# Performance work log

Measured on AMD Instinct MI355X. Metric: run time of the kernel, lower is better.

## Reference

```python
import jax, jax.numpy as jnp
import numpy as np

HIDDEN = 768
HEADS = 12
HEAD_DIM = HIDDEN // HEADS


def setup_inputs() -> dict:
    key = jax.random.key(0)
    ks = jax.random.split(key, 5)
    B, S = 1, 4096
    scale = 1.0 / np.sqrt(HIDDEN)
    return {
        "x": jax.random.normal(ks[0], (B, S, HIDDEN), dtype=jnp.float32),
        "w_qkv": jax.random.normal(ks[1], (HIDDEN, 3 * HIDDEN), dtype=jnp.float32) * scale,
        "b_qkv": jnp.zeros((3 * HIDDEN,), dtype=jnp.float32),
        "w_proj": jax.random.normal(ks[2], (HIDDEN, HIDDEN), dtype=jnp.float32) * scale,
        "b_proj": jnp.zeros((HIDDEN,), dtype=jnp.float32),
    }


def reference(x, w_qkv, b_qkv, w_proj, b_proj):
    B, S, D = x.shape
    H, Hd = HEADS, HEAD_DIM
    qkv = x @ w_qkv + b_qkv                        # [B,S,3D]
    qkv = qkv.reshape(B, S, 3, H, Hd)
    q, k, v = (jnp.moveaxis(qkv[:, :, i], 2, 1) for i in range(3))  # [B,H,S,Hd]
    scale = 1.0 / np.sqrt(Hd)
    attn = jnp.einsum("bhqd,bhkd->bhqk", q, k) * scale
    attn = jax.nn.softmax(attn, axis=-1)
    o = jnp.einsum("bhqk,bhkd->bhqd", attn, v)     # [B,H,S,Hd]
    o = jnp.moveaxis(o, 1, 2).reshape(B, S, D)
    return o @ w_proj + b_proj
```

## Files before the change

### kernel.cpp

```cpp
#include <hip/hip_runtime.h>

#define S_LEN 4096
#define DMODEL 768
#define NHEAD 12
#define HDIM 64
#define DQKV 2304

typedef __attribute__((ext_vector_type(8))) __bf16 bf16x8;
typedef __attribute__((ext_vector_type(4))) float f32x4;
typedef __attribute__((ext_vector_type(8))) unsigned short ushort8;

#define LOG2E 1.4426950408889634f

#if __has_builtin(__builtin_amdgcn_exp2f)
#define EXP2(x) __builtin_amdgcn_exp2f(x)
#else
#define EXP2(x) exp2f(x)
#endif

static __device__ __forceinline__ unsigned short f2bf(float f) {
  unsigned int u = __float_as_uint(f);
  u += 0x7FFFu + ((u >> 16) & 1u);
  return (unsigned short)(u >> 16);
}

static __device__ __forceinline__ void gload_lds16(const unsigned short* g, unsigned short* l) {
  __builtin_amdgcn_global_load_lds(
      (const __attribute__((address_space(1))) unsigned int*)g,
      (__attribute__((address_space(3))) unsigned int*)l, 16, 0, 0);
}

__global__ __launch_bounds__(256) void k_convert(const float* __restrict__ in,
                                                 unsigned short* __restrict__ out,
                                                 int n) {
  int i = (blockIdx.x * 256 + threadIdx.x) * 8;
  if (i >= n) return;
  const float4* p = reinterpret_cast<const float4*>(in + i);
  float4 a = p[0], b = p[1];
  ushort8 r;
  r[0] = f2bf(a.x); r[1] = f2bf(a.y); r[2] = f2bf(a.z); r[3] = f2bf(a.w);
  r[4] = f2bf(b.x); r[5] = f2bf(b.y); r[6] = f2bf(b.z); r[7] = f2bf(b.w);
  *reinterpret_cast<ushort8*>(out + i) = r;
}

__global__ __launch_bounds__(256) void k_transpose(const float* __restrict__ in,
                                                   unsigned short* __restrict__ out,
                                                   int Kdim, int Ndim) {
  __shared__ unsigned short t[64 * 65];
  int k0 = blockIdx.y * 64, n0 = blockIdx.x * 64;
  int tid = threadIdx.x;
#pragma unroll
  for (int p = 0; p < 4; ++p) {
    int r = p * 16 + (tid >> 4);
    int c = (tid & 15) * 4;
    float4 v = *reinterpret_cast<const float4*>(in + (size_t)(k0 + r) * Ndim + n0 + c);
    t[(c + 0) * 65 + r] = f2bf(v.x);
    t[(c + 1) * 65 + r] = f2bf(v.y);
    t[(c + 2) * 65 + r] = f2bf(v.z);
    t[(c + 3) * 65 + r] = f2bf(v.w);
  }
  __syncthreads();
#pragma unroll
  for (int p = 0; p < 2; ++p) {
    int task = p * 256 + tid;
    int rr = task >> 3;
    int cc = (task & 7) * 8;
    ushort8 r;
#pragma unroll
    for (int j = 0; j < 8; ++j) r[j] = t[rr * 65 + cc + j];
    *reinterpret_cast<ushort8*>(out + (size_t)(n0 + rr) * Kdim + k0 + cc) = r;
  }
}

template <int MODE>
__global__ __launch_bounds__(256) void k_gemm(const unsigned short* __restrict__ A,
                                              const unsigned short* __restrict__ Bt,
                                              const float* __restrict__ bias,
                                              unsigned short* __restrict__ Qb,
                                              unsigned short* __restrict__ Kf,
                                              unsigned short* __restrict__ Vf,
                                              float* __restrict__ outf) {
  __shared__ unsigned short As[2][128 * 32];
  __shared__ unsigned short Bs[2][128 * 32];

  int tid = threadIdx.x;
  int lane = tid & 63, wave = tid >> 6;
  int wr = wave >> 1, wc = wave & 1;
  int m0 = blockIdx.y * 128, n0 = blockIdx.x * 128;
  int r16 = lane & 15, g = lane >> 4;

  int ca0 = wave * 2, ca1 = wave * 2 + 1;
  int srow = lane >> 2, scol = (lane & 3) * 8;

  f32x4 acc[4][4] = {};

#define GSTAGE(BUF, K0)                                                                 \
  do {                                                                                  \
    gload_lds16(A + (size_t)(m0 + ca0 * 16 + srow) * DMODEL + (K0) + scol,              \
                &As[BUF][ca0 * 512]);                                                   \
    gload_lds16(A + (size_t)(m0 + ca1 * 16 + srow) * DMODEL + (K0) + scol,              \
                &As[BUF][ca1 * 512]);                                                   \
    gload_lds16(Bt + (size_t)(n0 + ca0 * 16 + srow) * DMODEL + (K0) + scol,             \
                &Bs[BUF][ca0 * 512]);                                                   \
    gload_lds16(Bt + (size_t)(n0 + ca1 * 16 + srow) * DMODEL + (K0) + scol,             \
                &Bs[BUF][ca1 * 512]);                                                   \
  } while (0)

  GSTAGE(0, 0);
  for (int kt = 0; kt < DMODEL / 32; ++kt) {
    int cur = kt & 1;
    __syncthreads();

    bf16x8 af[4], bfr[4];
#pragma unroll
    for (int m = 0; m < 4; ++m)
      af[m] = *reinterpret_cast<const bf16x8*>(&As[cur][(wr * 64 + m * 16 + r16) * 32 + g * 8]);
#pragma unroll
    for (int n = 0; n < 4; ++n)
      bfr[n] = *reinterpret_cast<const bf16x8*>(&Bs[cur][(wc * 64 + n * 16 + r16) * 32 + g * 8]);

    if (kt < DMODEL / 32 - 1) GSTAGE(cur ^ 1, (kt + 1) * 32);

#pragma unroll
    for (int m = 0; m < 4; ++m)
#pragma unroll
      for (int n = 0; n < 4; ++n)
        acc[m][n] = __builtin_amdgcn_mfma_f32_16x16x32_bf16(af[m], bfr[n], acc[m][n], 0, 0, 0);
  }
#undef GSTAGE

#pragma unroll
  for (int m = 0; m < 4; ++m) {
    int grow0 = m0 + wr * 64 + m * 16 + 4 * g;
#pragma unroll
    for (int n = 0; n < 4; ++n) {
      int gcol = n0 + wc * 64 + n * 16 + r16;
      float bv = bias[gcol];
      if (MODE == 0) {
        int sect = gcol / DMODEL;
        int rem = gcol - sect * DMODEL;
        int h = rem >> 6, hd = rem & 63;
        if (sect == 2) {
          int j = hd >> 4, r16v = hd & 15;
          int tile = grow0 >> 6, kk = (grow0 >> 5) & 1, g2 = (grow0 >> 3) & 3, e0 = grow0 & 7;
          size_t base = (((size_t)h * 64 + tile) * 8 + (j * 2 + kk)) * 512 +
                        (size_t)(g2 * 16 + r16v) * 8 + e0;
          ushort4 pk;
          pk.x = f2bf(acc[m][n][0] + bv);
          pk.y = f2bf(acc[m][n][1] + bv);
          pk.z = f2bf(acc[m][n][2] + bv);
          pk.w = f2bf(acc[m][n][3] + bv);
          *reinterpret_cast<ushort4*>(Vf + base) = pk;
        } else if (sect == 0) {
#pragma unroll
          for (int i = 0; i < 4; ++i)
            Qb[((size_t)h * S_LEN + grow0 + i) * HDIM + hd] =
                f2bf((acc[m][n][i] + bv) * (0.125f * LOG2E));
        } else {
          int kk = hd >> 5, g2 = (hd >> 3) & 3, e = hd & 7;
#pragma unroll
          for (int i = 0; i < 4; ++i) {
            int s = grow0 + i;
            int tile = s >> 6, r = s & 63;
            int j = (((r >> 2) & 1) << 1) | (r >> 5);
            int r16l = (r & 3) | (((r >> 3) & 3) << 2);
            size_t idx = (((size_t)h * 64 + tile) * 8 + (j * 2 + kk)) * 512 +
                         (size_t)(g2 * 16 + r16l) * 8 + e;
            Kf[idx] = f2bf(acc[m][n][i] + bv);
          }
        }
      } else {
#pragma unroll
        for (int i = 0; i < 4; ++i)
          outf[(size_t)(grow0 + i) * DMODEL + gcol] = acc[m][n][i] + bv;
      }
    }
  }
}

__global__ __launch_bounds__(256, 3) void k_attn(const unsigned short* __restrict__ Q,
                                                 const unsigned short* __restrict__ Kf,
                                                 const unsigned short* __restrict__ Vf,
                                                 float* __restrict__ Opart,
                                                 float* __restrict__ Lpart,
                                                 float* __restrict__ Mpart) {
  __shared__ unsigned short ldsK[2][4096];
  __shared__ unsigned short ldsV[2][4096];

  int tid = threadIdx.x;
  int lane = tid & 63, wave = tid >> 6;
  int r16 = lane & 15, g = lane >> 4;

  int bid = blockIdx.x;
  int gid = (bid & 7) * 96 + (bid >> 3);
  int h = gid >> 6;
  int rem = gid & 63;
  int half = rem & 1;
  int qb = rem >> 1;
  int qbaseA = qb * 128 + wave * 16;
  int qbaseB = qbaseA + 64;
  int tb = half * 32;

  const unsigned short* KfH = Kf + (size_t)h * (64 * 4096);
  const unsigned short* VfH = Vf + (size_t)h * (64 * 4096);
  float* OpH = Opart + ((size_t)half * NHEAD + h) * S_LEN * HDIM;
  float* LpH = Lpart + ((size_t)half * NHEAD + h) * S_LEN;
  float* MpH = Mpart + ((size_t)half * NHEAD + h) * S_LEN;

  const unsigned short* qpA = Q + ((size_t)h * S_LEN + qbaseA + r16) * HDIM + g * 8;
  const unsigned short* qpB = Q + ((size_t)h * S_LEN + qbaseB + r16) * HDIM + g * 8;
  bf16x8 qf0a = *reinterpret_cast<const bf16x8*>(qpA);
  bf16x8 qf1a = *reinterpret_cast<const bf16x8*>(qpA + 32);
  bf16x8 qf0b = *reinterpret_cast<const bf16x8*>(qpB);
  bf16x8 qf1b = *reinterpret_cast<const bf16x8*>(qpB + 32);

  f32x4 oaccA[4] = {}, oaccB[4] = {};
  f32x4 lsumA = {}, lsumB = {};
  f32x4 zinitA = {}, zinitB = {};
  float mrowA = 0.f, mrowB = 0.f;
  bf16x8 bones;
#pragma unroll
  for (int e = 0; e < 8; ++e) bones[e] = (__bf16)1.0f;

  int c0 = wave, c1 = wave + 4;

#define STAGE(BUF, T)                                                        \
  do {                                                                       \
    const unsigned short* kg_ = KfH + (size_t)(T) * 4096;                    \
    const unsigned short* vg_ = VfH + (size_t)(T) * 4096;                    \
    gload_lds16(kg_ + c0 * 512 + lane * 8, &ldsK[BUF][c0 * 512]);            \
    gload_lds16(kg_ + c1 * 512 + lane * 8, &ldsK[BUF][c1 * 512]);            \
    gload_lds16(vg_ + c0 * 512 + lane * 8, &ldsV[BUF][c0 * 512]);            \
    gload_lds16(vg_ + c1 * 512 + lane * 8, &ldsV[BUF][c1 * 512]);            \
  } while (0)

#define QK(SARR, QF0, QF1, ZI)                                                          \
  do {                                                                                  \
    _Pragma("unroll") for (int j_ = 0; j_ < 4; ++j_) {                                  \
      f32x4 z_ = ZI;                                                                    \
      z_ = __builtin_amdgcn_mfma_f32_16x16x32_bf16(kfr_[2 * j_], QF0, z_, 0, 0, 0);     \
      SARR[j_] = __builtin_amdgcn_mfma_f32_16x16x32_bf16(kfr_[2 * j_ + 1], QF1, z_, 0, 0, 0); \
    }                                                                                   \
  } while (0)

#define SOFTPV(SARR, MROW, ZI, LSUM, OACC, FIRST)                                       \
  do {                                                                                  \
    float x1_ = fmaxf(fmaxf(SARR[0][0], SARR[0][1]), SARR[0][2]);                       \
    float x2_ = fmaxf(fmaxf(SARR[0][3], SARR[1][0]), SARR[1][1]);                       \
    float x3_ = fmaxf(fmaxf(SARR[1][2], SARR[1][3]), SARR[2][0]);                       \
    float x4_ = fmaxf(fmaxf(SARR[2][1], SARR[2][2]), SARR[2][3]);                       \
    float x5_ = fmaxf(fmaxf(SARR[3][0], SARR[3][1]), SARR[3][2]);                       \
    float pm_ = fmaxf(fmaxf(fmaxf(x1_, x2_), fmaxf(x3_, x4_)), fmaxf(x5_, SARR[3][3])); \
    pm_ = fmaxf(pm_, __shfl_xor(pm_, 16));                                              \
    pm_ = fmaxf(pm_, __shfl_xor(pm_, 32));                                              \
    if (FIRST) {                                                                        \
      _Pragma("unroll") for (int j_ = 0; j_ < 4; ++j_)                                  \
        _Pragma("unroll") for (int i_ = 0; i_ < 4; ++i_) SARR[j_][i_] -= pm_;           \
      MROW = pm_;                                                                       \
      ZI[0] = -MROW; ZI[1] = -MROW; ZI[2] = -MROW; ZI[3] = -MROW;                       \
    } else if (__any(pm_ > 8.f)) {                                                      \
      float dl_ = fmaxf(pm_, 0.f);                                                      \
      float al_ = EXP2(-dl_);                                                           \
      float a0_ = __shfl(al_, 20 * g + 0), a1_ = __shfl(al_, 20 * g + 1);               \
      float a2_ = __shfl(al_, 20 * g + 2), a3_ = __shfl(al_, 20 * g + 3);               \
      LSUM[0] *= a0_; LSUM[1] *= a1_; LSUM[2] *= a2_; LSUM[3] *= a3_;                   \
      _Pragma("unroll") for (int j_ = 0; j_ < 4; ++j_) {                                \
        OACC[j_][0] *= a0_; OACC[j_][1] *= a1_;                                         \
        OACC[j_][2] *= a2_; OACC[j_][3] *= a3_;                                         \
      }                                                                                 \
      _Pragma("unroll") for (int j_ = 0; j_ < 4; ++j_)                                  \
        _Pragma("unroll") for (int i_ = 0; i_ < 4; ++i_) SARR[j_][i_] -= dl_;           \
      MROW += dl_;                                                                      \
      ZI[0] = -MROW; ZI[1] = -MROW; ZI[2] = -MROW; ZI[3] = -MROW;                       \
    }                                                                                   \
    float p_[4][4];                                                                     \
    _Pragma("unroll") for (int j_ = 0; j_ < 4; ++j_)                                    \
      _Pragma("unroll") for (int i_ = 0; i_ < 4; ++i_)                                  \
        p_[j_][i_] = EXP2(SARR[j_][i_]);                                                \
    bf16x8 pa0_, pa1_;                                                                  \
    _Pragma("unroll") for (int e_ = 0; e_ < 8; ++e_) {                                  \
      pa0_[e_] = (__bf16)p_[2 * (e_ >> 2)][e_ & 3];                                     \
      pa1_[e_] = (__bf16)p_[1 + 2 * (e_ >> 2)][e_ & 3];                                 \
    }                                                                                   \
    LSUM = __builtin_amdgcn_mfma_f32_16x16x32_bf16(pa0_, bones, LSUM, 0, 0, 0);         \
    LSUM = __builtin_amdgcn_mfma_f32_16x16x32_bf16(pa1_, bones, LSUM, 0, 0, 0);         \
    _Pragma("unroll") for (int j_ = 0; j_ < 4; ++j_) {                                  \
      OACC[j_] = __builtin_amdgcn_mfma_f32_16x16x32_bf16(pa0_, vfr_[2 * j_], OACC[j_], 0, 0, 0); \
      OACC[j_] = __builtin_amdgcn_mfma_f32_16x16x32_bf16(pa1_, vfr_[2 * j_ + 1], OACC[j_], 0, 0, 0); \
    }                                                                                   \
  } while (0)

#define BODY(CUR, DO_STAGE, T, FIRSTF)                                                  \
  do {                                                                                  \
    __syncthreads();          \
    bf16x8 kfr_[8], vfr_[8];                                                            \
    _Pragma("unroll") for (int f_ = 0; f_ < 8; ++f_) {                                  \
      kfr_[f_] = *reinterpret_cast<const bf16x8*>(&ldsK[CUR][f_ * 512 + lane * 8]);     \
      vfr_[f_] = *reinterpret_cast<const bf16x8*>(&ldsV[CUR][f_ * 512 + lane * 8]);     \
    }                                                                                   \
    if (DO_STAGE) STAGE((CUR) ^ 1, (T) + 1);                                            \
    f32x4 sA_[4], sB_[4];                                                               \
    QK(sA_, qf0a, qf1a, zinitA);                                                        \
    QK(sB_, qf0b, qf1b, zinitB);                                                        \
    SOFTPV(sA_, mrowA, zinitA, lsumA, oaccA, FIRSTF);                                   \
    SOFTPV(sB_, mrowB, zinitB, lsumB, oaccB, FIRSTF);                                   \
  } while (0)

  STAGE(0, tb);
  BODY(0, true, tb, true);
  for (int pr = 0; pr < 15; ++pr) {
    BODY(1, true, tb + 2 * pr + 1, false);
    BODY(0, true, tb + 2 * pr + 2, false);
  }
  BODY(1, false, tb + 31, false);
#undef BODY
#undef SOFTPV
#undef QK
#undef STAGE

#pragma unroll
  for (int i = 0; i < 4; ++i) {
    int srowA = qbaseA + 4 * g + i;
    int srowB = qbaseB + 4 * g + i;
#pragma unroll
    for (int j = 0; j < 4; ++j) {
      int col = j * 16 + r16;
      OpH[(size_t)srowA * HDIM + col] = oaccA[j][i];
      OpH[(size_t)srowB * HDIM + col] = oaccB[j][i];
    }
  }
  if (g == 0) {
    MpH[qbaseA + r16] = mrowA;
    MpH[qbaseB + r16] = mrowB;
  }
  if (r16 == 0) {
#pragma unroll
    for (int i = 0; i < 4; ++i) {
      LpH[qbaseA + 4 * g + i] = lsumA[i];
      LpH[qbaseB + 4 * g + i] = lsumB[i];
    }
  }
}

__global__ __launch_bounds__(256) void k_combine(const float* __restrict__ Opart,
                                                 const float* __restrict__ Lpart,
                                                 const float* __restrict__ Mpart,
                                                 unsigned short* __restrict__ O) {
  int gidx = blockIdx.x * 256 + threadIdx.x;
  int h = gidx >> 15;
  int rem = gidx & 32767;
  int s = rem >> 3;
  int d0 = (rem & 7) * 8;
  size_t i0 = (size_t)h * S_LEN + s;
  size_t o0 = i0 * HDIM + d0;
  const size_t HS_O = (size_t)NHEAD * S_LEN * HDIM;
  const size_t HS_L = (size_t)NHEAD * S_LEN;

  float m0 = Mpart[i0], m1 = Mpart[HS_L + i0];
  float l0 = Lpart[i0], l1 = Lpart[HS_L + i0];
  float m = fmaxf(m0, m1);
  float w0 = EXP2(m0 - m), w1 = EXP2(m1 - m);
  float inv = 1.0f / (l0 * w0 + l1 * w1);
  float4 a0 = *reinterpret_cast<const float4*>(Opart + o0);
  float4 a1 = *reinterpret_cast<const float4*>(Opart + o0 + 4);
  float4 b0 = *reinterpret_cast<const float4*>(Opart + HS_O + o0);
  float4 b1 = *reinterpret_cast<const float4*>(Opart + HS_O + o0 + 4);
  ushort8 r;
  r[0] = f2bf((a0.x * w0 + b0.x * w1) * inv);
  r[1] = f2bf((a0.y * w0 + b0.y * w1) * inv);
  r[2] = f2bf((a0.z * w0 + b0.z * w1) * inv);
  r[3] = f2bf((a0.w * w0 + b0.w * w1) * inv);
  r[4] = f2bf((a1.x * w0 + b1.x * w1) * inv);
  r[5] = f2bf((a1.y * w0 + b1.y * w1) * inv);
  r[6] = f2bf((a1.z * w0 + b1.z * w1) * inv);
  r[7] = f2bf((a1.w * w0 + b1.w * w1) * inv);
  *reinterpret_cast<ushort8*>(O + (size_t)s * DMODEL + h * HDIM + d0) = r;
}

extern "C" void kernel_launch(void* const* d_in, const int* in_sizes, int n_in,
                              void* d_out, int out_size, void* d_ws, size_t ws_size,
                              hipStream_t stream) {
  const float* x = (const float*)d_in[0];
  const float* w_qkv = (const float*)d_in[1];
  const float* b_qkv = (const float*)d_in[2];
  const float* w_proj = (const float*)d_in[3];
  const float* b_proj = (const float*)d_in[4];
  float* out = (float*)d_out;

  unsigned short* ws16 = (unsigned short*)d_ws;
  unsigned short* xb = ws16;
  unsigned short* wqkvT = xb + (size_t)S_LEN * DMODEL;
  unsigned short* wprojT = wqkvT + (size_t)DQKV * DMODEL;
  unsigned short* Qb = wprojT + (size_t)DMODEL * DMODEL;
  unsigned short* Kf = Qb + (size_t)NHEAD * S_LEN * HDIM;
  unsigned short* Vf = Kf + (size_t)NHEAD * S_LEN * HDIM;
  float* Opart = (float*)(Vf + (size_t)NHEAD * S_LEN * HDIM);
  float* Lpart = Opart + (size_t)2 * NHEAD * S_LEN * HDIM;
  float* Mpart = Lpart + (size_t)2 * NHEAD * S_LEN;
  unsigned short* Ob = xb;

  k_convert<<<(S_LEN * DMODEL) / (256 * 8), 256, 0, stream>>>(x, xb, S_LEN * DMODEL);
  k_transpose<<<dim3(DQKV / 64, DMODEL / 64), 256, 0, stream>>>(w_qkv, wqkvT, DMODEL, DQKV);
  k_transpose<<<dim3(DMODEL / 64, DMODEL / 64), 256, 0, stream>>>(w_proj, wprojT, DMODEL, DMODEL);
  k_gemm<0><<<dim3(DQKV / 128, S_LEN / 128), 256, 0, stream>>>(xb, wqkvT, b_qkv, Qb, Kf, Vf, nullptr);
  k_attn<<<768, 256, 0, stream>>>(Qb, Kf, Vf, Opart, Lpart, Mpart);
  k_combine<<<(NHEAD * S_LEN * 8) / 256, 256, 0, stream>>>(Opart, Lpart, Mpart, Ob);
  k_gemm<1><<<dim3(DMODEL / 128, S_LEN / 128), 256, 0, stream>>>(Ob, wprojT, b_proj, nullptr, nullptr, nullptr, out);
}
```

Baseline: 131.2 us.

## Merge prep kernels, split attention KV into quarters, retile projection GEMM to 64x64

Three preprocessing launches (x convert and two weight transposes) become one kernel that dispatches on block index. The attention split-KV goes from 2 to 4 partitions, giving 1536 blocks for better CU occupancy, and the combine kernel now merges four partials. The output projection GEMM gets its own kernel with 64x64 tiles, so it launches 768 blocks instead of 192. The trade-off is more partial-output traffic and combine work, plus more workspace.

```diff
diff --git a/kernel.cpp b/kernel.cpp
--- a/kernel.cpp
+++ b/kernel.cpp
@@ -30,25 +30,38 @@
       (__attribute__((address_space(3))) unsigned int*)l, 16, 0, 0);
 }
 
-__global__ __launch_bounds__(256) void k_convert(const float* __restrict__ in,
-                                                 unsigned short* __restrict__ out,
-                                                 int n) {
-  int i = (blockIdx.x * 256 + threadIdx.x) * 8;
-  if (i >= n) return;
-  const float4* p = reinterpret_cast<const float4*>(in + i);
-  float4 a = p[0], b = p[1];
-  ushort8 r;
-  r[0] = f2bf(a.x); r[1] = f2bf(a.y); r[2] = f2bf(a.z); r[3] = f2bf(a.w);
-  r[4] = f2bf(b.x); r[5] = f2bf(b.y); r[6] = f2bf(b.z); r[7] = f2bf(b.w);
-  *reinterpret_cast<ushort8*>(out + i) = r;
-}
-
-__global__ __launch_bounds__(256) void k_transpose(const float* __restrict__ in,
-                                                   unsigned short* __restrict__ out,
-                                                   int Kdim, int Ndim) {
+__global__ __launch_bounds__(256) void k_prep(const float* __restrict__ x,
+                                              const float* __restrict__ w_qkv,
+                                              const float* __restrict__ w_proj,
+                                              unsigned short* __restrict__ xb,
+                                              unsigned short* __restrict__ wqkvT,
+                                              unsigned short* __restrict__ wprojT) {
   __shared__ unsigned short t[64 * 65];
-  int k0 = blockIdx.y * 64, n0 = blockIdx.x * 64;
+  int bid = blockIdx.x;
   int tid = threadIdx.x;
+  if (bid < 1536) {
+    int i = (bid * 256 + tid) * 8;
+    const float4* p = reinterpret_cast<const float4*>(x + i);
+    float4 a = p[0], b = p[1];
+    ushort8 r;
+    r[0] = f2bf(a.x); r[1] = f2bf(a.y); r[2] = f2bf(a.z); r[3] = f2bf(a.w);
+    r[4] = f2bf(b.x); r[5] = f2bf(b.y); r[6] = f2bf(b.z); r[7] = f2bf(b.w);
+    *reinterpret_cast<ushort8*>(xb + i) = r;
+    return;
+  }
+  const float* in;
+  unsigned short* out;
+  int Kdim, Ndim, bx, by;
+  if (bid < 1968) {
+    int tt = bid - 1536;
+    in = w_qkv; out = wqkvT; Kdim = DMODEL; Ndim = DQKV;
+    bx = tt % 36; by = tt / 36;
+  } else {
+    int tt = bid - 1968;
+    in = w_proj; out = wprojT; Kdim = DMODEL; Ndim = DMODEL;
+    bx = tt % 12; by = tt / 12;
+  }
+  int k0 = by * 64, n0 = bx * 64;
 #pragma unroll
   for (int p = 0; p < 4; ++p) {
     int r = p * 16 + (tid >> 4);
@@ -72,14 +85,12 @@
   }
 }
 
-template <int MODE>
-__global__ __launch_bounds__(256) void k_gemm(const unsigned short* __restrict__ A,
-                                              const unsigned short* __restrict__ Bt,
-                                              const float* __restrict__ bias,
-                                              unsigned short* __restrict__ Qb,
-                                              unsigned short* __restrict__ Kf,
-                                              unsigned short* __restrict__ Vf,
-                                              float* __restrict__ outf) {
+__global__ __launch_bounds__(256) void k_gemm_qkv(const unsigned short* __restrict__ A,
+                                                  const unsigned short* __restrict__ Bt,
+                                                  const float* __restrict__ bias,
+                                                  unsigned short* __restrict__ Qb,
+                                                  unsigned short* __restrict__ Kf,
+                                                  unsigned short* __restrict__ Vf) {
   __shared__ unsigned short As[2][128 * 32];
   __shared__ unsigned short Bs[2][128 * 32];
 
@@ -136,44 +147,99 @@
     for (int n = 0; n < 4; ++n) {
       int gcol = n0 + wc * 64 + n * 16 + r16;
       float bv = bias[gcol];
-      if (MODE == 0) {
-        int sect = gcol / DMODEL;
-        int rem = gcol - sect * DMODEL;
-        int h = rem >> 6, hd = rem & 63;
-        if (sect == 2) {
-          int j = hd >> 4, r16v = hd & 15;
-          int tile = grow0 >> 6, kk = (grow0 >> 5) & 1, g2 = (grow0 >> 3) & 3, e0 = grow0 & 7;
-          size_t base = (((size_t)h * 64 + tile) * 8 + (j * 2 + kk)) * 512 +
-                        (size_t)(g2 * 16 + r16v) * 8 + e0;
-          ushort4 pk;
-          pk.x = f2bf(acc[m][n][0] + bv);
-          pk.y = f2bf(acc[m][n][1] + bv);
-          pk.z = f2bf(acc[m][n][2] + bv);
-          pk.w = f2bf(acc[m][n][3] + bv);
-          *reinterpret_cast<ushort4*>(Vf + base) = pk;
-        } else if (sect == 0) {
-#pragma unroll
-          for (int i = 0; i < 4; ++i)
-            Qb[((size_t)h * S_LEN + grow0 + i) * HDIM + hd] =
-                f2bf((acc[m][n][i] + bv) * (0.125f * LOG2E));
-        } else {
-          int kk = hd >> 5, g2 = (hd >> 3) & 3, e = hd & 7;
-#pragma unroll
-          for (int i = 0; i < 4; ++i) {
-            int s = grow0 + i;
-            int tile = s >> 6, r = s & 63;
-            int j = (((r >> 2) & 1) << 1) | (r >> 5);
-            int r16l = (r & 3) | (((r >> 3) & 3) << 2);
-            size_t idx = (((size_t)h * 64 + tile) * 8 + (j * 2 + kk)) * 512 +
-                         (size_t)(g2 * 16 + r16l) * 8 + e;
-            Kf[idx] = f2bf(acc[m][n][i] + bv);
-          }
+      int sect = gcol / DMODEL;
+      int rem = gcol - sect * DMODEL;
+      int h = rem >> 6, hd = rem & 63;
+      if (sect == 2) {
+        int j = hd >> 4, r16v = hd & 15;
+        int tile = grow0 >> 6, kk = (grow0 >> 5) & 1, g2 = (grow0 >> 3) & 3, e0 = grow0 & 7;
+        size_t base = (((size_t)h * 64 + tile) * 8 + (j * 2 + kk)) * 512 +
+                      (size_t)(g2 * 16 + r16v) * 8 + e0;
+        ushort4 pk;
+        pk.x = f2bf(acc[m][n][0] + bv);
+        pk.y = f2bf(acc[m][n][1] + bv);
+        pk.z = f2bf(acc[m][n][2] + bv);
+        pk.w = f2bf(acc[m][n][3] + bv);
+        *reinterpret_cast<ushort4*>(Vf + base) = pk;
+      } else if (sect == 0) {
+#pragma unroll
+        for (int i = 0; i < 4; ++i)
+          Qb[((size_t)h * S_LEN + grow0 + i) * HDIM + hd] =
+              f2bf((acc[m][n][i] + bv) * (0.125f * LOG2E));
+      } else {
+        int kk = hd >> 5, g2 = (hd >> 3) & 3, e = hd & 7;
+#pragma unroll
+        for (int i = 0; i < 4; ++i) {
+          int s = grow0 + i;
+          int tile = s >> 6, r = s & 63;
+          int j = (((r >> 2) & 1) << 1) | (r >> 5);
+          int r16l = (r & 3) | (((r >> 3) & 3) << 2);
+          size_t idx = (((size_t)h * 64 + tile) * 8 + (j * 2 + kk)) * 512 +
+                       (size_t)(g2 * 16 + r16l) * 8 + e;
+          Kf[idx] = f2bf(acc[m][n][i] + bv);
         }
-      } else {
-#pragma unroll
-        for (int i = 0; i < 4; ++i)
-          outf[(size_t)(grow0 + i) * DMODEL + gcol] = acc[m][n][i] + bv;
       }
+    }
+  }
+}
+
+__global__ __launch_bounds__(256) void k_gemm_proj(const unsigned short* __restrict__ A,
+                                                   const unsigned short* __restrict__ Bt,
+                                                   const float* __restrict__ bias,
+                                                   float* __restrict__ outf) {
+  __shared__ unsigned short As[2][64 * 32];
+  __shared__ unsigned short Bs[2][64 * 32];
+
+  int tid = threadIdx.x;
+  int lane = tid & 63, wave = tid >> 6;
+  int wr = wave >> 1, wc = wave & 1;
+  int m0 = blockIdx.y * 64, n0 = blockIdx.x * 64;
+  int r16 = lane & 15, g = lane >> 4;
+  int srow = lane >> 2, scol = (lane & 3) * 8;
+
+  f32x4 acc[2][2] = {};
+
+#define GSTAGE(BUF, K0)                                                                 \
+  do {                                                                                  \
+    gload_lds16(A + (size_t)(m0 + wave * 16 + srow) * DMODEL + (K0) + scol,             \
+                &As[BUF][wave * 512]);                                                  \
+    gload_lds16(Bt + (size_t)(n0 + wave * 16 + srow) * DMODEL + (K0) + scol,            \
+                &Bs[BUF][wave * 512]);                                                  \
+  } while (0)
+
+  GSTAGE(0, 0);
+  for (int kt = 0; kt < DMODEL / 32; ++kt) {
+    int cur = kt & 1;
+    __syncthreads();
+
+    bf16x8 af[2], bfr[2];
+#pragma unroll
+    for (int m = 0; m < 2; ++m)
+      af[m] = *reinterpret_cast<const bf16x8*>(&As[cur][(wr * 32 + m * 16 + r16) * 32 + g * 8]);
+#pragma unroll
+    for (int n = 0; n < 2; ++n)
+      bfr[n] = *reinterpret_cast<const bf16x8*>(&Bs[cur][(wc * 32 + n * 16 + r16) * 32 + g * 8]);
+
+    if (kt < DMODEL / 32 - 1) GSTAGE(cur ^ 1, (kt + 1) * 32);
+
+#pragma unroll
+    for (int m = 0; m < 2; ++m)
+#pragma unroll
+      for (int n = 0; n < 2; ++n)
+        acc[m][n] = __builtin_amdgcn_mfma_f32_16x16x32_bf16(af[m], bfr[n], acc[m][n], 0, 0, 0);
+  }
+#undef GSTAGE
+
+#pragma unroll
+  for (int m = 0; m < 2; ++m) {
+    int grow0 = m0 + wr * 32 + m * 16 + 4 * g;
+#pragma unroll
+    for (int n = 0; n < 2; ++n) {
+      int gcol = n0 + wc * 32 + n * 16 + r16;
+      float bv = bias[gcol];
+#pragma unroll
+      for (int i = 0; i < 4; ++i)
+        outf[(size_t)(grow0 + i) * DMODEL + gcol] = acc[m][n][i] + bv;
     }
   }
 }
@@ -192,20 +258,20 @@
   int r16 = lane & 15, g = lane >> 4;
 
   int bid = blockIdx.x;
-  int gid = (bid & 7) * 96 + (bid >> 3);
-  int h = gid >> 6;
-  int rem = gid & 63;
-  int half = rem & 1;
-  int qb = rem >> 1;
+  int gid = (bid & 7) * 192 + (bid >> 3);
+  int h = gid >> 7;
+  int rem = gid & 127;
+  int quarter = rem & 3;
+  int qb = rem >> 2;
   int qbaseA = qb * 128 + wave * 16;
   int qbaseB = qbaseA + 64;
-  int tb = half * 32;
+  int tb = quarter * 16;
 
   const unsigned short* KfH = Kf + (size_t)h * (64 * 4096);
   const unsigned short* VfH = Vf + (size_t)h * (64 * 4096);
-  float* OpH = Opart + ((size_t)half * NHEAD + h) * S_LEN * HDIM;
-  float* LpH = Lpart + ((size_t)half * NHEAD + h) * S_LEN;
-  float* MpH = Mpart + ((size_t)half * NHEAD + h) * S_LEN;
+  float* OpH = Opart + ((size_t)quarter * NHEAD + h) * S_LEN * HDIM;
+  float* LpH = Lpart + ((size_t)quarter * NHEAD + h) * S_LEN;
+  float* MpH = Mpart + ((size_t)quarter * NHEAD + h) * S_LEN;
 
   const unsigned short* qpA = Q + ((size_t)h * S_LEN + qbaseA + r16) * HDIM + g * 8;
   const unsigned short* qpB = Q + ((size_t)h * S_LEN + qbaseB + r16) * HDIM + g * 8;
@@ -292,7 +358,7 @@
 
 #define BODY(CUR, DO_STAGE, T, FIRSTF)                                                  \
   do {                                                                                  \
-    __syncthreads();          \
+    __syncthreads();                                                                    \
     bf16x8 kfr_[8], vfr_[8];                                                            \
     _Pragma("unroll") for (int f_ = 0; f_ < 8; ++f_) {                                  \
       kfr_[f_] = *reinterpret_cast<const bf16x8*>(&ldsK[CUR][f_ * 512 + lane * 8]);     \
@@ -308,11 +374,11 @@
 
   STAGE(0, tb);
   BODY(0, true, tb, true);
-  for (int pr = 0; pr < 15; ++pr) {
+  for (int pr = 0; pr < 7; ++pr) {
     BODY(1, true, tb + 2 * pr + 1, false);
     BODY(0, true, tb + 2 * pr + 2, false);
   }
-  BODY(1, false, tb + 31, false);
+  BODY(1, false, tb + 15, false);
 #undef BODY
 #undef SOFTPV
 #undef QK
@@ -357,23 +423,31 @@
   const size_t HS_L = (size_t)NHEAD * S_LEN;
 
   float m0 = Mpart[i0], m1 = Mpart[HS_L + i0];
+  float m2 = Mpart[2 * HS_L + i0], m3 = Mpart[3 * HS_L + i0];
   float l0 = Lpart[i0], l1 = Lpart[HS_L + i0];
-  float m = fmaxf(m0, m1);
-  float w0 = EXP2(m0 - m), w1 = EXP2(m1 - m);
-  float inv = 1.0f / (l0 * w0 + l1 * w1);
-  float4 a0 = *reinterpret_cast<const float4*>(Opart + o0);
-  float4 a1 = *reinterpret_cast<const float4*>(Opart + o0 + 4);
-  float4 b0 = *reinterpret_cast<const float4*>(Opart + HS_O + o0);
-  float4 b1 = *reinterpret_cast<const float4*>(Opart + HS_O + o0 + 4);
+  float l2 = Lpart[2 * HS_L + i0], l3 = Lpart[3 * HS_L + i0];
+  float m = fmaxf(fmaxf(m0, m1), fmaxf(m2, m3));
+  float w0 = EXP2(m0 - m), w1 = EXP2(m1 - m), w2 = EXP2(m2 - m), w3 = EXP2(m3 - m);
+  float inv = 1.0f / (l0 * w0 + l1 * w1 + l2 * w2 + l3 * w3);
+
+  float acc[8];
+#pragma unroll
+  for (int q = 0; q < 4; ++q) {
+    float w = (q == 0) ? w0 : (q == 1) ? w1 : (q == 2) ? w2 : w3;
+    const float* src = Opart + q * HS_O + o0;
+    float4 a = *reinterpret_cast<const float4*>(src);
+    float4 b = *reinterpret_cast<const float4*>(src + 4);
+    if (q == 0) {
+      acc[0] = a.x * w; acc[1] = a.y * w; acc[2] = a.z * w; acc[3] = a.w * w;
+      acc[4] = b.x * w; acc[5] = b.y * w; acc[6] = b.z * w; acc[7] = b.w * w;
+    } else {
+      acc[0] += a.x * w; acc[1] += a.y * w; acc[2] += a.z * w; acc[3] += a.w * w;
+      acc[4] += b.x * w; acc[5] += b.y * w; acc[6] += b.z * w; acc[7] += b.w * w;
+    }
+  }
   ushort8 r;
-  r[0] = f2bf((a0.x * w0 + b0.x * w1) * inv);
-  r[1] = f2bf((a0.y * w0 + b0.y * w1) * inv);
-  r[2] = f2bf((a0.z * w0 + b0.z * w1) * inv);
-  r[3] = f2bf((a0.w * w0 + b0.w * w1) * inv);
-  r[4] = f2bf((a1.x * w0 + b1.x * w1) * inv);
-  r[5] = f2bf((a1.y * w0 + b1.y * w1) * inv);
-  r[6] = f2bf((a1.z * w0 + b1.z * w1) * inv);
-  r[7] = f2bf((a1.w * w0 + b1.w * w1) * inv);
+#pragma unroll
+  for (int e = 0; e < 8; ++e) r[e] = f2bf(acc[e] * inv);
   *reinterpret_cast<ushort8*>(O + (size_t)s * DMODEL + h * HDIM + d0) = r;
 }
 
@@ -395,15 +469,13 @@
   unsigned short* Kf = Qb + (size_t)NHEAD * S_LEN * HDIM;
   unsigned short* Vf = Kf + (size_t)NHEAD * S_LEN * HDIM;
   float* Opart = (float*)(Vf + (size_t)NHEAD * S_LEN * HDIM);
-  float* Lpart = Opart + (size_t)2 * NHEAD * S_LEN * HDIM;
-  float* Mpart = Lpart + (size_t)2 * NHEAD * S_LEN;
+  float* Lpart = Opart + (size_t)4 * NHEAD * S_LEN * HDIM;
+  float* Mpart = Lpart + (size_t)4 * NHEAD * S_LEN;
   unsigned short* Ob = xb;
 
-  k_convert<<<(S_LEN * DMODEL) / (256 * 8), 256, 0, stream>>>(x, xb, S_LEN * DMODEL);
-  k_transpose<<<dim3(DQKV / 64, DMODEL / 64), 256, 0, stream>>>(w_qkv, wqkvT, DMODEL, DQKV);
-  k_transpose<<<dim3(DMODEL / 64, DMODEL / 64), 256, 0, stream>>>(w_proj, wprojT, DMODEL, DMODEL);
-  k_gemm<0><<<dim3(DQKV / 128, S_LEN / 128), 256, 0, stream>>>(xb, wqkvT, b_qkv, Qb, Kf, Vf, nullptr);
-  k_attn<<<768, 256, 0, stream>>>(Qb, Kf, Vf, Opart, Lpart, Mpart);
+  k_prep<<<2112, 256, 0, stream>>>(x, w_qkv, w_proj, xb, wqkvT, wprojT);
+  k_gemm_qkv<<<dim3(DQKV / 128, S_LEN / 128), 256, 0, stream>>>(xb, wqkvT, b_qkv, Qb, Kf, Vf);
+  k_attn<<<1536, 256, 0, stream>>>(Qb, Kf, Vf, Opart, Lpart, Mpart);
   k_combine<<<(NHEAD * S_LEN * 8) / 256, 256, 0, stream>>>(Opart, Lpart, Mpart, Ob);
-  k_gemm<1><<<dim3(DMODEL / 128, S_LEN / 128), 256, 0, stream>>>(Ob, wprojT, b_proj, nullptr, nullptr, nullptr, out);
-}
+  k_gemm_proj<<<dim3(DMODEL / 64, S_LEN / 64), 256, 0, stream>>>(Ob, wprojT, b_proj, out);
+}
```

After: 126.6 us. 1.04x faster.
